# Kernel optimization log

Measured on AMD Instinct MI355X. Metric: run time of the kernel, lower is better.

## Reference

```python
import jax, jax.numpy as jnp
import numpy as np

N_NODES = 50000


def gcn_conv(x, W, b, src, dst, n_nodes):
    # Linear transform first (PyG GCNConv): [N, out]
    h = x @ W
    # Add self-loops
    loop = jnp.arange(n_nodes, dtype=src.dtype)
    s = jnp.concatenate([src, loop])
    d = jnp.concatenate([dst, loop])
    # Symmetric normalization: deg counted at destination with unit weights
    deg = jax.ops.segment_sum(jnp.ones_like(d, dtype=h.dtype), d, num_segments=n_nodes)
    dinv = jnp.where(deg > 0, jax.lax.rsqrt(deg), 0.0)
    norm = dinv[s] * dinv[d]  # [E+N]
    # Gather source features, scale, scatter-add to destinations
    msgs = h[s] * norm[:, None]
    out = jax.ops.segment_sum(msgs, d, num_segments=n_nodes)
    return out + b


def setup_inputs() -> dict:
    key = jax.random.key(0)
    k1, k2, k3, k4, k5 = jax.random.split(key, 5)
    in_c, out_c = 512, 128
    x = jax.random.normal(k1, (N_NODES, in_c), dtype=jnp.float32)
    edge_index = jax.random.randint(k2, (2, 800000), 0, N_NODES, dtype=jnp.int64)
    glorot = 1.0 / np.sqrt(in_c)
    W_mu = jax.random.uniform(k3, (in_c, out_c), jnp.float32, -glorot, glorot)
    W_logstd = jax.random.uniform(k4, (in_c, out_c), jnp.float32, -glorot, glorot)
    b_mu = jnp.zeros((out_c,), jnp.float32)
    b_logstd = jnp.zeros((out_c,), jnp.float32)
    return {"x": x, "edge_index": edge_index, "W_mu": W_mu, "b_mu": b_mu,
            "W_logstd": W_logstd, "b_logstd": b_logstd}


def reference(x, edge_index, W_mu, b_mu, W_logstd, b_logstd):
    src, dst = edge_index[0], edge_index[1]
    mu = gcn_conv(x, W_mu, b_mu, src, dst, N_NODES)
    logstd = gcn_conv(x, W_logstd, b_logstd, src, dst, N_NODES)
    return mu, logstd
```

## Files before the change

### kernel.cpp

```cpp
#include <hip/hip_runtime.h>

#define NN 50000
#define NE 800000
#define KC 512
#define OC 256
#define NB_SCAN 196

typedef float f32x4 __attribute__((ext_vector_type(4)));
typedef short bf16x8 __attribute__((ext_vector_type(8)));

__device__ __forceinline__ unsigned f2bf(float f) {
    union { float f; unsigned u; } v; v.f = f;
    return (v.u + 0x7FFFu + ((v.u >> 16) & 1u)) >> 16;
}
__device__ __forceinline__ float bf2f(unsigned short b) {
    union { unsigned u; float f; } v; v.u = ((unsigned)b) << 16;
    return v.f;
}

__global__ __launch_bounds__(256) void count_deg_kernel(const int* __restrict__ ei,
                                                        int* __restrict__ deg) {
    int e = blockIdx.x * 256 + threadIdx.x;
    if (e < NE) atomicAdd(&deg[ei[NE + e]], 1);
}

__global__ __launch_bounds__(256) void scan_part_kernel(const int* __restrict__ deg,
                                                        int* __restrict__ partial) {
    int tid = threadIdx.x;
    int i = blockIdx.x * 256 + tid;
    int v = (i < NN) ? deg[i] : 0;
#pragma unroll
    for (int off = 32; off > 0; off >>= 1) v += __shfl_down(v, off, 64);
    __shared__ int wsum[4];
    if ((tid & 63) == 0) wsum[tid >> 6] = v;
    __syncthreads();
    if (tid == 0) partial[blockIdx.x] = wsum[0] + wsum[1] + wsum[2] + wsum[3];
}

__global__ __launch_bounds__(256) void scan_block_kernel(const int* __restrict__ partial,
                                                         int* __restrict__ blockoff) {
    __shared__ int lds[256];
    int tid = threadIdx.x;
    int v = (tid < NB_SCAN) ? partial[tid] : 0;
    lds[tid] = v;
    __syncthreads();
    for (int off = 1; off < 256; off <<= 1) {
        int t = (tid >= off) ? lds[tid - off] : 0;
        __syncthreads();
        lds[tid] += t;
        __syncthreads();
    }
    if (tid < NB_SCAN) blockoff[tid] = lds[tid] - v;
}

__global__ __launch_bounds__(256) void scan_apply_kernel(const int* __restrict__ deg,
                                                         const int* __restrict__ blockoff,
                                                         int* __restrict__ row_start,
                                                         int* __restrict__ cursor,
                                                         float* __restrict__ dinv) {
    int tid = threadIdx.x;
    int lane = tid & 63;
    int w = tid >> 6;
    int i = blockIdx.x * 256 + tid;
    int d = (i < NN) ? deg[i] : 0;
    int v = d;
#pragma unroll
    for (int off = 1; off < 64; off <<= 1) {
        int t = __shfl_up(v, off, 64);
        if (lane >= off) v += t;
    }
    __shared__ int wsum[4];
    if (lane == 63) wsum[w] = v;
    __syncthreads();
    int wof = 0;
    for (int k = 0; k < w; ++k) wof += wsum[k];
    int excl = blockoff[blockIdx.x] + wof + v - d;
    if (i < NN) {
        row_start[i] = excl;
        cursor[i] = excl;
        dinv[i] = rsqrtf((float)(d + 1));
    }
    if (i == NN - 1) row_start[NN] = excl + d;
}

__global__ __launch_bounds__(256) void scatter_kernel(const int* __restrict__ ei,
                                                      int* __restrict__ cursor,
                                                      int* __restrict__ csr_src) {
    int e = blockIdx.x * 256 + threadIdx.x;
    if (e < NE) {
        int d = ei[NE + e];
        int pos = atomicAdd(&cursor[d], 1);
        csr_src[pos] = ei[e];
    }
}

__global__ __launch_bounds__(256) void convw_kernel(const float* __restrict__ Wmu,
                                                    const float* __restrict__ Wls,
                                                    uint4* __restrict__ Wc) {
    int idx = blockIdx.x * 256 + threadIdx.x;
    int u = idx & 1023;
    int kb = idx >> 10;
    int s = u ^ ((u >> 3) & 7);
    int col = s >> 2;
    int g = s & 3;
    int k0 = kb * 32 + g * 8;
    const float* Wsrc = (col < 128) ? (Wmu + col) : (Wls + (col - 128));
    unsigned o[4];
#pragma unroll
    for (int p = 0; p < 4; ++p) {
        float lo = Wsrc[(size_t)(k0 + 2 * p) * 128];
        float hi = Wsrc[(size_t)(k0 + 2 * p + 1) * 128];
        o[p] = f2bf(lo) | (f2bf(hi) << 16);
    }
    uint4 v;
    v.x = o[0]; v.y = o[1]; v.z = o[2]; v.w = o[3];
    Wc[idx] = v;
}

__global__ __launch_bounds__(256) void gemm_kernel(const float* __restrict__ x,
                                                   const uint4* __restrict__ Wc,
                                                   const float* __restrict__ dinv,
                                                   unsigned short* __restrict__ hs) {
    __shared__ __align__(16) unsigned short As[2][64 * 40];
    __shared__ __align__(16) unsigned short Bs[2][1024 * 8];

    int tid = threadIdx.x;
    int lane = tid & 63;
    int w = tid >> 6;
    int r0 = blockIdx.x * 64;

    int st_row = tid >> 2;
    int st_g = tid & 3;
    int xr = r0 + st_row;
    if (xr > NN - 1) xr = NN - 1;
    const float* xg = x + (size_t)xr * KC + st_g * 8;

    f32x4 acc[4][4];
    f32x4 zz = {0.f, 0.f, 0.f, 0.f};
#pragma unroll
    for (int a = 0; a < 4; ++a)
#pragma unroll
        for (int b = 0; b < 4; ++b) acc[a][b] = zz;

    float4 a0, a1;
    uint4 b0, b1, b2, b3;

    auto loadAB = [&](int kb) {
        a0 = *(const float4*)(xg + kb * 32);
        a1 = *(const float4*)(xg + kb * 32 + 4);
        const uint4* wsrc = Wc + kb * 1024 + tid;
        b0 = wsrc[0];
        b1 = wsrc[256];
        b2 = wsrc[512];
        b3 = wsrc[768];
    };
    auto storeAB = [&](int buf) {
        uint4 av;
        av.x = f2bf(a0.x) | (f2bf(a0.y) << 16);
        av.y = f2bf(a0.z) | (f2bf(a0.w) << 16);
        av.z = f2bf(a1.x) | (f2bf(a1.y) << 16);
        av.w = f2bf(a1.z) | (f2bf(a1.w) << 16);
        *(uint4*)&As[buf][st_row * 40 + st_g * 8] = av;
        uint4* bd = (uint4*)&Bs[buf][0];
        bd[tid] = b0;
        bd[tid + 256] = b1;
        bd[tid + 512] = b2;
        bd[tid + 768] = b3;
    };

    int i16 = lane & 15;
    int g4 = lane >> 4;

    loadAB(0);
    storeAB(0);
    __syncthreads();

#pragma unroll 2
    for (int kb = 0; kb < 16; ++kb) {
        int buf = kb & 1;
        if (kb < 15) loadAB(kb + 1);

        bf16x8 af[4];
#pragma unroll
        for (int fr = 0; fr < 4; ++fr)
            af[fr] = *(const bf16x8*)&As[buf][(fr * 16 + i16) * 40 + g4 * 8];
#pragma unroll
        for (int fc = 0; fc < 4; ++fc) {
            int scol = ((w * 64 + fc * 16 + i16) << 2) + g4;
            int u = scol ^ ((scol >> 3) & 7);
            bf16x8 bfrag = *(const bf16x8*)&Bs[buf][u * 8];
#pragma unroll
            for (int fr = 0; fr < 4; ++fr)
                acc[fr][fc] = __builtin_amdgcn_mfma_f32_16x16x32_bf16(af[fr], bfrag, acc[fr][fc], 0, 0, 0);
        }

        if (kb < 15) storeAB(buf ^ 1);
        __syncthreads();
    }

#pragma unroll
    for (int fr = 0; fr < 4; ++fr) {
#pragma unroll
        for (int r = 0; r < 4; ++r) {
            int gr = r0 + fr * 16 + g4 * 4 + r;
            if (gr < NN) {
                float dv = dinv[gr];
#pragma unroll
                for (int fc = 0; fc < 4; ++fc) {
                    int col = w * 64 + fc * 16 + i16;
                    hs[(size_t)gr * OC + col] = (unsigned short)f2bf(acc[fr][fc][r] * dv);
                }
            }
        }
    }
}

__global__ __launch_bounds__(256) void aggregate_kernel(const unsigned short* __restrict__ hs,
                                                        const int* __restrict__ row_start,
                                                        const int* __restrict__ csr_src,
                                                        const float* __restrict__ dinv,
                                                        const float* __restrict__ bmu,
                                                        const float* __restrict__ bls,
                                                        float* __restrict__ out) {
    int tid = threadIdx.x;
    int lane = tid & 63;
    int node = blockIdx.x * 4 + (tid >> 6);

    const unsigned short* hrow = hs + lane * 4;
    float acc0, acc1, acc2, acc3;
    {
        ushort4 v = *(const ushort4*)&hrow[(size_t)node * OC];
        acc0 = bf2f(v.x);
        acc1 = bf2f(v.y);
        acc2 = bf2f(v.z);
        acc3 = bf2f(v.w);
    }
    int rs = row_start[node], re = row_start[node + 1];
    int e = rs;
    for (; e + 8 <= re; e += 8) {
        int s[8];
#pragma unroll
        for (int q = 0; q < 8; ++q) s[q] = csr_src[e + q];
        ushort4 v[8];
#pragma unroll
        for (int q = 0; q < 8; ++q) v[q] = *(const ushort4*)&hrow[(size_t)s[q] * OC];
#pragma unroll
        for (int q = 0; q < 8; ++q) {
            acc0 += bf2f(v[q].x);
            acc1 += bf2f(v[q].y);
            acc2 += bf2f(v[q].z);
            acc3 += bf2f(v[q].w);
        }
    }
    if (e + 4 <= re) {
        int s[4];
#pragma unroll
        for (int q = 0; q < 4; ++q) s[q] = csr_src[e + q];
        ushort4 v[4];
#pragma unroll
        for (int q = 0; q < 4; ++q) v[q] = *(const ushort4*)&hrow[(size_t)s[q] * OC];
#pragma unroll
        for (int q = 0; q < 4; ++q) {
            acc0 += bf2f(v[q].x);
            acc1 += bf2f(v[q].y);
            acc2 += bf2f(v[q].z);
            acc3 += bf2f(v[q].w);
        }
        e += 4;
    }
    for (; e < re; ++e) {
        int s0 = csr_src[e];
        ushort4 v0 = *(const ushort4*)&hrow[(size_t)s0 * OC];
        acc0 += bf2f(v0.x);
        acc1 += bf2f(v0.y);
        acc2 += bf2f(v0.z);
        acc3 += bf2f(v0.w);
    }
    float dn = dinv[node];
    if (lane < 32) {
        float4 b = ((const float4*)bmu)[lane];
        float4 r = {acc0 * dn + b.x, acc1 * dn + b.y, acc2 * dn + b.z, acc3 * dn + b.w};
        ((float4*)out)[(size_t)node * 32 + lane] = r;
    } else {
        float4 b = ((const float4*)bls)[lane - 32];
        float4 r = {acc0 * dn + b.x, acc1 * dn + b.y, acc2 * dn + b.z, acc3 * dn + b.w};
        ((float4*)out)[(size_t)(NN + node) * 32 + (lane - 32)] = r;
    }
}

extern "C" void kernel_launch(void* const* d_in, const int* in_sizes, int n_in,
                              void* d_out, int out_size, void* d_ws, size_t ws_size,
                              hipStream_t stream) {
    const float* x = (const float*)d_in[0];
    const int* ei = (const int*)d_in[1];
    const float* Wmu = (const float*)d_in[2];
    const float* bmu = (const float*)d_in[3];
    const float* Wls = (const float*)d_in[4];
    const float* bls = (const float*)d_in[5];
    float* out = (float*)d_out;

    char* ws = (char*)d_ws;
    size_t off = 0;
    auto alloc = [&](size_t bytes) {
        void* p = ws + off;
        off += (bytes + 255) & ~(size_t)255;
        return p;
    };
    unsigned short* hs = (unsigned short*)alloc((size_t)NN * OC * sizeof(unsigned short));
    uint4* Wc = (uint4*)alloc((size_t)16384 * 16);
    int* deg = (int*)alloc((size_t)NN * sizeof(int));
    int* row_start = (int*)alloc((size_t)(NN + 1) * sizeof(int));
    int* cursor = (int*)alloc((size_t)NN * sizeof(int));
    int* csr_src = (int*)alloc((size_t)NE * sizeof(int));
    float* dinv = (float*)alloc((size_t)NN * sizeof(float));
    int* partial = (int*)alloc((size_t)NB_SCAN * sizeof(int));
    int* blockoff = (int*)alloc((size_t)NB_SCAN * sizeof(int));

    hipMemsetAsync(deg, 0, (size_t)NN * sizeof(int), stream);

    count_deg_kernel<<<(NE + 255) / 256, 256, 0, stream>>>(ei, deg);
    scan_part_kernel<<<NB_SCAN, 256, 0, stream>>>(deg, partial);
    scan_block_kernel<<<1, 256, 0, stream>>>(partial, blockoff);
    scan_apply_kernel<<<NB_SCAN, 256, 0, stream>>>(deg, blockoff, row_start, cursor, dinv);
    scatter_kernel<<<(NE + 255) / 256, 256, 0, stream>>>(ei, cursor, csr_src);
    convw_kernel<<<64, 256, 0, stream>>>(Wmu, Wls, Wc);
    gemm_kernel<<<(NN + 63) / 64, 256, 0, stream>>>(x, Wc, dinv, hs);
    aggregate_kernel<<<NN / 4, 256, 0, stream>>>(hs, row_start, csr_src, dinv, bmu, bls, out);
}
```

Baseline: 198.9 us.

## Load W fragments directly to registers and stage larger A chunks in LDS

The GEMM kernel stops staging the converted weight matrix in shared memory. Wc is re-laid out per wave and lane so each wave loads its MFMA B fragments straight from global memory into double-buffered registers. The x tile is now staged in 128-wide K chunks, which cuts block-wide barriers from sixteen to three. The trade is more register pressure and per-wave redundant global/L2 reads of W in place of shared-memory reuse.

```diff
diff --git a/kernel.cpp b/kernel.cpp
--- a/kernel.cpp
+++ b/kernel.cpp
@@ -98,12 +98,14 @@
                                                     const float* __restrict__ Wls,
                                                     uint4* __restrict__ Wc) {
     int idx = blockIdx.x * 256 + threadIdx.x;
-    int u = idx & 1023;
     int kb = idx >> 10;
-    int s = u ^ ((u >> 3) & 7);
-    int col = s >> 2;
-    int g = s & 3;
-    int k0 = kb * 32 + g * 8;
+    int rem = idx & 1023;
+    int wf = rem >> 6;
+    int lane = rem & 63;
+    int g4 = lane >> 4;
+    int i16 = lane & 15;
+    int col = (wf >> 2) * 64 + (wf & 3) * 16 + i16;
+    int k0 = kb * 32 + g4 * 8;
     const float* Wsrc = (col < 128) ? (Wmu + col) : (Wls + (col - 128));
     unsigned o[4];
 #pragma unroll
@@ -117,23 +119,51 @@
     Wc[idx] = v;
 }
 
+#define ALD 136
 __global__ __launch_bounds__(256) void gemm_kernel(const float* __restrict__ x,
                                                    const uint4* __restrict__ Wc,
                                                    const float* __restrict__ dinv,
                                                    unsigned short* __restrict__ hs) {
-    __shared__ __align__(16) unsigned short As[2][64 * 40];
-    __shared__ __align__(16) unsigned short Bs[2][1024 * 8];
+    __shared__ __align__(16) unsigned short As[2][64 * ALD];
 
     int tid = threadIdx.x;
     int lane = tid & 63;
     int w = tid >> 6;
     int r0 = blockIdx.x * 64;
+    int i16 = lane & 15;
+    int g4 = lane >> 4;
 
     int st_row = tid >> 2;
-    int st_g = tid & 3;
+    int st_c = tid & 3;
     int xr = r0 + st_row;
     if (xr > NN - 1) xr = NN - 1;
-    const float* xg = x + (size_t)xr * KC + st_g * 8;
+    const float* xg = x + (size_t)xr * KC + st_c * 32;
+    unsigned short* adst = &As[0][st_row * ALD + st_c * 32];
+
+    float4 xa[8];
+    auto loadA = [&](int S) {
+#pragma unroll
+        for (int i = 0; i < 8; ++i) xa[i] = *(const float4*)(xg + S * 128 + i * 4);
+    };
+    auto storeA = [&](int buf) {
+        uint4* dst = (uint4*)(adst + buf * 64 * ALD);
+#pragma unroll
+        for (int p = 0; p < 4; ++p) {
+            uint4 o;
+            o.x = f2bf(xa[2 * p].x) | (f2bf(xa[2 * p].y) << 16);
+            o.y = f2bf(xa[2 * p].z) | (f2bf(xa[2 * p].w) << 16);
+            o.z = f2bf(xa[2 * p + 1].x) | (f2bf(xa[2 * p + 1].y) << 16);
+            o.w = f2bf(xa[2 * p + 1].z) | (f2bf(xa[2 * p + 1].w) << 16);
+            dst[p] = o;
+        }
+    };
+
+    const uint4* wbase = Wc + (size_t)(w * 4) * 64 + lane;
+    uint4 bb[2][4];
+    auto loadB = [&](int dbuf, int kb) {
+#pragma unroll
+        for (int fc = 0; fc < 4; ++fc) bb[dbuf][fc] = wbase[kb * 1024 + fc * 64];
+    };
 
     f32x4 acc[4][4];
     f32x4 zz = {0.f, 0.f, 0.f, 0.f};
@@ -142,60 +172,36 @@
 #pragma unroll
         for (int b = 0; b < 4; ++b) acc[a][b] = zz;
 
-    float4 a0, a1;
-    uint4 b0, b1, b2, b3;
-
-    auto loadAB = [&](int kb) {
-        a0 = *(const float4*)(xg + kb * 32);
-        a1 = *(const float4*)(xg + kb * 32 + 4);
-        const uint4* wsrc = Wc + kb * 1024 + tid;
-        b0 = wsrc[0];
-        b1 = wsrc[256];
-        b2 = wsrc[512];
-        b3 = wsrc[768];
-    };
-    auto storeAB = [&](int buf) {
-        uint4 av;
-        av.x = f2bf(a0.x) | (f2bf(a0.y) << 16);
-        av.y = f2bf(a0.z) | (f2bf(a0.w) << 16);
-        av.z = f2bf(a1.x) | (f2bf(a1.y) << 16);
-        av.w = f2bf(a1.z) | (f2bf(a1.w) << 16);
-        *(uint4*)&As[buf][st_row * 40 + st_g * 8] = av;
-        uint4* bd = (uint4*)&Bs[buf][0];
-        bd[tid] = b0;
-        bd[tid + 256] = b1;
-        bd[tid + 512] = b2;
-        bd[tid + 768] = b3;
-    };
-
-    int i16 = lane & 15;
-    int g4 = lane >> 4;
-
-    loadAB(0);
-    storeAB(0);
+    loadA(0);
+    storeA(0);
     __syncthreads();
-
-#pragma unroll 2
-    for (int kb = 0; kb < 16; ++kb) {
-        int buf = kb & 1;
-        if (kb < 15) loadAB(kb + 1);
-
-        bf16x8 af[4];
-#pragma unroll
-        for (int fr = 0; fr < 4; ++fr)
-            af[fr] = *(const bf16x8*)&As[buf][(fr * 16 + i16) * 40 + g4 * 8];
-#pragma unroll
-        for (int fc = 0; fc < 4; ++fc) {
-            int scol = ((w * 64 + fc * 16 + i16) << 2) + g4;
-            int u = scol ^ ((scol >> 3) & 7);
-            bf16x8 bfrag = *(const bf16x8*)&Bs[buf][u * 8];
+    loadA(1);
+    loadB(0, 0);
+
+#pragma unroll
+    for (int S = 0; S < 4; ++S) {
+#pragma unroll
+        for (int ks = 0; ks < 4; ++ks) {
+            const int kb = S * 4 + ks;
+            const int cur = kb & 1;
+            if (kb < 15) loadB(cur ^ 1, kb + 1);
+            bf16x8 af[4];
 #pragma unroll
             for (int fr = 0; fr < 4; ++fr)
-                acc[fr][fc] = __builtin_amdgcn_mfma_f32_16x16x32_bf16(af[fr], bfrag, acc[fr][fc], 0, 0, 0);
-        }
-
-        if (kb < 15) storeAB(buf ^ 1);
-        __syncthreads();
+                af[fr] = *(const bf16x8*)&As[S & 1][(fr * 16 + i16) * ALD + ks * 32 + g4 * 8];
+#pragma unroll
+            for (int fc = 0; fc < 4; ++fc) {
+                bf16x8 bfrag = *(const bf16x8*)&bb[cur][fc];
+#pragma unroll
+                for (int fr = 0; fr < 4; ++fr)
+                    acc[fr][fc] = __builtin_amdgcn_mfma_f32_16x16x32_bf16(af[fr], bfrag, acc[fr][fc], 0, 0, 0);
+            }
+        }
+        if (S < 3) {
+            storeA((S + 1) & 1);
+            __syncthreads();
+            if (S < 2) loadA(S + 2);
+        }
     }
 
 #pragma unroll
```

Measured after the change: 203.9 us. 1.03x slower.
